# Performance work log

Hardware: AMD Instinct MI355X
Metric: run time of the kernel (lower is better)

Reference implementation:

```python
import jax, jax.numpy as jnp
import numpy as np

H, N, DIN, DOUT = 8, 2048, 768, 1024
HD = DOUT // H
SCALE = 1.0 / float(np.sqrt(HD))
NEG = -1e9
EPS = 1e-5


def setup_inputs() -> dict:
    key = jax.random.key(0)
    ks = jax.random.split(key, 20)
    w = lambda i, shape: jax.random.normal(ks[i], shape, jnp.float32) * 0.02
    inp = {
        'x': jax.random.normal(ks[0], (N, DIN), jnp.float32),
        'batch': jnp.sort(jax.random.randint(ks[1], (N,), 0, 64)).astype(jnp.int64)
                 if jax.config.jax_enable_x64 else jnp.sort(jax.random.randint(ks[1], (N,), 0, 64)),
        'motif_to_atom_attn': jax.random.normal(ks[2], (H, N, N), jnp.float32),
        'wq_w': w(3, (DIN, DOUT)), 'wq_b': jnp.zeros((DOUT,), jnp.float32),
        'wk_w': w(4, (DIN, DOUT)), 'wk_b': jnp.zeros((DOUT,), jnp.float32),
        'wv_w': w(5, (DIN, DOUT)), 'wv_b': jnp.zeros((DOUT,), jnp.float32),
        'wo_w': w(6, (DOUT, DIN)), 'wo_b': jnp.zeros((DIN,), jnp.float32),
        'ln_g': jnp.ones((DIN,), jnp.float32), 'ln_b': jnp.zeros((DIN,), jnp.float32),
        'alpha': jnp.float32(0.5), 'beta': jnp.float32(0.5),
        'gate_q_w': w(7, (DOUT, H)), 'gate_q_b': jnp.zeros((H,), jnp.float32),
        'gate_k_w': w(8, (DOUT, H)), 'gate_k_b': jnp.zeros((H,), jnp.float32),
        'head_interaction': jnp.eye(H, dtype=jnp.float32) + 0.01 * jax.random.normal(ks[9], (H, H), jnp.float32),
    }
    return inp


def reference(x, batch, motif_to_atom_attn, wq_w, wq_b, wk_w, wk_b, wv_w, wv_b,
              wo_w, wo_b, ln_g, ln_b, alpha, beta, gate_q_w, gate_q_b,
              gate_k_w, gate_k_b, head_interaction):
    n = x.shape[0]
    # projections -> [H, N, hd]
    q = (x @ wq_w + wq_b).reshape(n, H, HD).transpose(1, 0, 2)
    k = (x @ wk_w + wk_b).reshape(n, H, HD).transpose(1, 0, 2)
    v = (x @ wv_w + wv_b).reshape(n, H, HD).transpose(1, 0, 2)
    # scaled scores with block-diagonal batch mask [H, N, N]
    scores = jnp.einsum('hid,hjd->hij', q, k) * SCALE
    mask = batch[:, None] == batch[None, :]
    scores = jnp.where(mask[None, :, :], scores, NEG)
    attn_final = scores
    # Guide bias: torch permutes (N,N,H)->permute(2,1,0) which TRANSPOSES node dims
    attn_base = alpha * scores + beta * motif_to_atom_attn          # [H, N, N]
    attn_final = attn_final + jnp.swapaxes(attn_base, 1, 2)        # transposed in (i,j)
    # dynamic gating
    q_flat = q.transpose(1, 0, 2).reshape(n, DOUT)
    k_flat = k.transpose(1, 0, 2).reshape(n, DOUT)
    gq = jnp.tanh(q_flat @ gate_q_w + gate_q_b)                    # [N, H]
    gk = jnp.tanh(k_flat @ gate_k_w + gate_k_b)                    # [N, H]
    attn_final = attn_final + scores * (gq.T[:, :, None] + gk.T[:, None, :])
    # head interaction: res[m,i,j] = sum_h scores[h,i,j] * W[h,m]
    attn_final = attn_final + jnp.einsum('hij,hm->mij', scores, head_interaction)
    probs = jax.nn.softmax(attn_final, axis=-1)
    out = jnp.einsum('hij,hjd->hid', probs, v).transpose(1, 0, 2).reshape(n, DOUT)
    out = out @ wo_w + wo_b
    y = out + x
    mu = jnp.mean(y, axis=-1, keepdims=True)
    var = jnp.mean(jnp.square(y - mu), axis=-1, keepdims=True)
    y = (y - mu) * jax.lax.rsqrt(var + EPS) * ln_g + ln_b
    return y, attn_final
```

## Files before the change

kernel.cpp:

```cpp
#include <hip/hip_runtime.h>

#define NN    2048
#define DIN   768
#define DOUT  1024
#define NH    8
#define HD    128
#define SCALEF 0.08838834764831845f
#define NEGF  (-1.0e9f)
#define EPSF  1e-5f
#define EXPSHIFT 16.0f

typedef __attribute__((ext_vector_type(4))) float f32x4;
typedef __attribute__((ext_vector_type(8))) short bf16x8;

#define OFF_OBF  0
#define OFF_WOT  1048576
#define OFF_YACC 1441792
#define OFF_Q    3686400
#define OFF_K    4734976
#define OFF_VB   5783552
#define OFF_VT   6832128
#define OFF_XB   7880704
#define OFF_WT   8667136
#define OFF_GQ   9846784
#define OFF_GK   9863168

__device__ __forceinline__ short f2bf(float f) {
  union { float f; unsigned u; } v; v.f = f;
  unsigned r = v.u + 0x7FFF + ((v.u >> 16) & 1);
  return (short)(r >> 16);
}
__device__ __forceinline__ float bf2f(short s) {
  union { unsigned u; float f; } v; v.u = ((unsigned)(unsigned short)s) << 16;
  return v.f;
}

__global__ __launch_bounds__(256) void k_prep(const float* __restrict__ x,
                                              short* __restrict__ xb,
                                              const float* __restrict__ wq,
                                              const float* __restrict__ wk,
                                              const float* __restrict__ wv,
                                              short* __restrict__ Wt,
                                              const float* __restrict__ wo,
                                              short* __restrict__ wot) {
  const int bid = blockIdx.x;
  const int tid = threadIdx.x;
  if (bid < 1536) {
    int idx = bid * 256 + tid;
    float4 v = ((const float4*)x)[idx];
    union { short s[4]; float2 f; } u;
    u.s[0] = f2bf(v.x); u.s[1] = f2bf(v.y); u.s[2] = f2bf(v.z); u.s[3] = f2bf(v.w);
    ((float2*)xb)[idx] = u.f;
    return;
  }
  __shared__ float t[64][65];
  if (bid < 2112) {
    const int w = bid - 1536;
    const int z = w / 192, rem = w % 192;
    const int c0 = (rem % 16) * 64, k0 = (rem / 16) * 64;
    const float* Wm = (z == 0) ? wq : (z == 1) ? wk : wv;
#pragma unroll
    for (int l = 0; l < 4; ++l) {
      int f = tid + l * 256;
      int r = f >> 4, c4 = (f & 15) * 4;
      *(float4*)&t[r][c4] = *(const float4*)(Wm + (size_t)(k0 + r) * DOUT + c0 + c4);
    }
    __syncthreads();
    int r2 = tid >> 2, q = tid & 3;
    union { short s[16]; float4 f[2]; } buf;
#pragma unroll
    for (int jj = 0; jj < 16; ++jj) buf.s[jj] = f2bf(t[q * 16 + jj][r2]);
    short* dst = Wt + (size_t)z * (1024 * 768) + (size_t)(c0 + r2) * 768 + k0 + q * 16;
    ((float4*)dst)[0] = buf.f[0];
    ((float4*)dst)[1] = buf.f[1];
  } else {
    const int w = bid - 2112;
    const int c0 = (w % 12) * 64, k0 = (w / 12) * 64;
#pragma unroll
    for (int l = 0; l < 4; ++l) {
      int f = tid + l * 256;
      int r = f >> 4, c4 = (f & 15) * 4;
      *(float4*)&t[r][c4] = *(const float4*)(wo + (size_t)(k0 + r) * DIN + c0 + c4);
    }
    __syncthreads();
    int r2 = tid >> 2, q = tid & 3;
    union { short s[16]; float4 f[2]; } buf;
#pragma unroll
    for (int jj = 0; jj < 16; ++jj) buf.s[jj] = f2bf(t[q * 16 + jj][r2]);
    short* dst = wot + (size_t)(c0 + r2) * DOUT + k0 + q * 16;
    ((float4*)dst)[0] = buf.f[0];
    ((float4*)dst)[1] = buf.f[1];
  }
}

__global__ __launch_bounds__(256) void k_qkv(const short* __restrict__ xb,
                                             const short* __restrict__ Wt,
                                             const float* __restrict__ bq,
                                             const float* __restrict__ bk,
                                             const float* __restrict__ bv,
                                             short* __restrict__ Qb,
                                             short* __restrict__ Kb,
                                             short* __restrict__ Vb) {
  const int n0 = blockIdx.x * 128;
  const int i0 = blockIdx.y * 64;
  const int mat = n0 >> 10;
  const int cl = n0 & 1023;
  const float* bias = (mat == 0) ? bq : (mat == 1) ? bk : bv;
  const short* Wm = Wt + (size_t)mat * (1024 * 768);
  const int tid = threadIdx.x, lane = tid & 63, wave = tid >> 6;
  const int ln = lane & 15, quad = lane >> 4, q8 = quad * 8;
  __shared__ __align__(16) short Bs[2][128][56];
  const int brow = tid >> 1, bseg = (tid & 1) * 16;
  const short* gB = Wm + (size_t)(cl + brow) * DIN + bseg;
  {
    bf16x8 b0 = *(const bf16x8*)(gB);
    bf16x8 b1 = *(const bf16x8*)(gB + 8);
    *(bf16x8*)&Bs[0][brow][bseg] = b0;
    *(bf16x8*)&Bs[0][brow][bseg + 8] = b1;
  }
  bf16x8 cb0 = *(const bf16x8*)(gB + 32);
  bf16x8 cb1 = *(const bf16x8*)(gB + 40);
  __syncthreads();
  f32x4 acc[8];
#pragma unroll
  for (int nt = 0; nt < 8; ++nt) acc[nt] = (f32x4){0.f, 0.f, 0.f, 0.f};
  const short* a0 = xb + (size_t)(i0 + 16 * wave + ln) * DIN + q8;
  for (int ks = 0; ks < 24; ++ks) {
    const int bufc = ks & 1;
    bf16x8 nb0, nb1;
    if (ks < 22) {
      nb0 = *(const bf16x8*)(gB + 32 * (ks + 2));
      nb1 = *(const bf16x8*)(gB + 32 * (ks + 2) + 8);
    }
    bf16x8 A0 = *(const bf16x8*)(a0 + 32 * ks);
#pragma unroll
    for (int nt = 0; nt < 8; ++nt) {
      bf16x8 B = *(const bf16x8*)&Bs[bufc][16 * nt + ln][q8];
      acc[nt] = __builtin_amdgcn_mfma_f32_16x16x32_bf16(A0, B, acc[nt], 0, 0, 0);
    }
    if (ks < 23) {
      *(bf16x8*)&Bs[bufc ^ 1][brow][bseg] = cb0;
      *(bf16x8*)&Bs[bufc ^ 1][brow][bseg + 8] = cb1;
    }
    __syncthreads();
    if (ks < 22) { cb0 = nb0; cb1 = nb1; }
  }
#pragma unroll
  for (int nt = 0; nt < 8; ++nt) {
    int cg = cl + 16 * nt + ln;
    float bb = bias[cg];
#pragma unroll
    for (int reg = 0; reg < 4; ++reg) {
      int rr = i0 + 16 * wave + quad * 4 + reg;
      short s = f2bf(acc[nt][reg] + bb);
      if (mat == 2) {
        Vb[(size_t)rr * 1024 + cg] = s;
      } else {
        int h = cg >> 7, d = cg & 127;
        (mat == 0 ? Qb : Kb)[((size_t)h * NN + rr) * HD + d] = s;
      }
    }
  }
}

__global__ __launch_bounds__(256) void k_vtg(const short* __restrict__ Qb,
                                             const short* __restrict__ Kb,
                                             const float* __restrict__ gqw,
                                             const float* __restrict__ gqb,
                                             const float* __restrict__ gkw,
                                             const float* __restrict__ gkb,
                                             float* __restrict__ GQ,
                                             float* __restrict__ GK,
                                             const short* __restrict__ Vb,
                                             short* __restrict__ Vt) {
  const int bid = blockIdx.x;
  const int tid = threadIdx.x;
  __shared__ __align__(16) char smem[17408];
  if (bid < 2048) {
    const int i = bid;
    const int lane = tid & 63, wave = tid >> 6;
    float aq[NH] = {}, ak[NH] = {};
    for (int d = tid; d < DOUT; d += 256) {
      int h = d >> 7, dd = d & 127;
      float qv = bf2f(Qb[((size_t)h * NN + i) * HD + dd]);
      float kv = bf2f(Kb[((size_t)h * NN + i) * HD + dd]);
      float4 ga = *(const float4*)(gqw + (size_t)d * NH);
      float4 gb = *(const float4*)(gqw + (size_t)d * NH + 4);
      float4 ha = *(const float4*)(gkw + (size_t)d * NH);
      float4 hb = *(const float4*)(gkw + (size_t)d * NH + 4);
      aq[0] = fmaf(qv, ga.x, aq[0]); aq[1] = fmaf(qv, ga.y, aq[1]);
      aq[2] = fmaf(qv, ga.z, aq[2]); aq[3] = fmaf(qv, ga.w, aq[3]);
      aq[4] = fmaf(qv, gb.x, aq[4]); aq[5] = fmaf(qv, gb.y, aq[5]);
      aq[6] = fmaf(qv, gb.z, aq[6]); aq[7] = fmaf(qv, gb.w, aq[7]);
      ak[0] = fmaf(kv, ha.x, ak[0]); ak[1] = fmaf(kv, ha.y, ak[1]);
      ak[2] = fmaf(kv, ha.z, ak[2]); ak[3] = fmaf(kv, ha.w, ak[3]);
      ak[4] = fmaf(kv, hb.x, ak[4]); ak[5] = fmaf(kv, hb.y, ak[5]);
      ak[6] = fmaf(kv, hb.z, ak[6]); ak[7] = fmaf(kv, hb.w, ak[7]);
    }
#pragma unroll
    for (int h = 0; h < NH; ++h) {
#pragma unroll
      for (int off = 1; off < 64; off <<= 1) {
        aq[h] += __shfl_xor(aq[h], off);
        ak[h] += __shfl_xor(ak[h], off);
      }
    }
    auto part = (float (*)[16])(smem);
    if (lane == 0) {
#pragma unroll
      for (int h = 0; h < NH; ++h) {
        part[wave][h] = aq[h];
        part[wave][8 + h] = ak[h];
      }
    }
    __syncthreads();
    if (tid < 16) {
      float s = part[0][tid] + part[1][tid] + part[2][tid] + part[3][tid];
      if (tid < 8) GQ[(size_t)i * NH + tid] = tanhf(s + gqb[tid]);
      else GK[(size_t)i * NH + tid - 8] = tanhf(s + gkb[tid - 8]);
    }
  } else {
    auto t = (short (*)[136])(smem);
    const int w = bid - 2048;
    const int i0 = (w & 31) * 64, h = w >> 5;
#pragma unroll
    for (int l = 0; l < 2; ++l) {
      int f = tid + l * 256;
      int r = f >> 3, c8 = (f & 7) * 16;
      const short* src = Vb + (size_t)(i0 + r) * 1024 + h * HD + c8;
      *(bf16x8*)&t[r][c8] = *(const bf16x8*)src;
      *(bf16x8*)&t[r][c8 + 8] = *(const bf16x8*)(src + 8);
    }
    __syncthreads();
    int d = tid >> 1, half = tid & 1;
    union { short s[32]; float4 f[4]; } buf;
#pragma unroll
    for (int ii = 0; ii < 32; ++ii) buf.s[ii] = t[32 * half + ii][d];
    short* dst = Vt + (size_t)h * (HD * NN) + (size_t)d * NN + i0 + 32 * half;
#pragma unroll
    for (int q = 0; q < 4; ++q) ((float4*)dst)[q] = buf.f[q];
  }
}

__global__ __launch_bounds__(256, 4) void k_sa(const short* __restrict__ Qb,
                                               const short* __restrict__ Kb,
                                               const int* __restrict__ batch,
                                               const float* __restrict__ motif,
                                               const float* __restrict__ GQ,
                                               const float* __restrict__ GK,
                                               const float* __restrict__ Wh,
                                               const float* __restrict__ alpha_p,
                                               const float* __restrict__ beta_p,
                                               float* __restrict__ ATTN) {
  const unsigned gid = blockIdx.y * gridDim.x + blockIdx.x;
  const unsigned xcd = gid & 7, idx = gid >> 3;
  const unsigned P = xcd + 8 * (idx >> 8);
  const unsigned r256 = idx & 255;
  const unsigned bx = 16 * (P & 3) + (r256 & 15);
  const unsigned by = 16 * (P >> 2) + (r256 >> 4);
  const int i0 = by * 32, j0 = bx * 32;

  const int tid = threadIdx.x, lane = tid & 63, wave = tid >> 6;
  const int wr = wave >> 1, wc = wave & 1;
  const int ln = lane & 15, quad = lane >> 4, q8 = quad * 8;

  __shared__ __align__(16) char smem[38400];
  auto Qs  = (short (*)[32][136])(smem);
  auto Ks  = (short (*)[32][136])(smem + 17408);
  auto oL  = (float (*)[36])(smem);
  auto gqL = (float (*)[12])(smem + 34816);
  auto gkL = (float (*)[12])(smem + 36352);
  float* sW = (float*)(smem + 37888);

  const int rA = 16 * wr + quad * 4;
  const int cA = 16 * wc + ln;

  const int srow = tid >> 3, sseg = (tid & 7) * 16;
  const short* gQ0 = Qb + (size_t)(i0 + srow) * HD + sseg;
  const short* gK0 = Kb + (size_t)(j0 + srow) * HD + sseg;
  const size_t hstep = (size_t)NN * HD;

  {
    bf16x8 q0 = *(const bf16x8*)(gQ0);
    bf16x8 q1 = *(const bf16x8*)(gQ0 + 8);
    bf16x8 k0 = *(const bf16x8*)(gK0);
    bf16x8 k1 = *(const bf16x8*)(gK0 + 8);
    *(bf16x8*)&Qs[0][srow][sseg] = q0;
    *(bf16x8*)&Qs[0][srow][sseg + 8] = q1;
    *(bf16x8*)&Ks[0][srow][sseg] = k0;
    *(bf16x8*)&Ks[0][srow][sseg + 8] = k1;
  }
  bf16x8 cq0 = *(const bf16x8*)(gQ0 + hstep);
  bf16x8 cq1 = *(const bf16x8*)(gQ0 + hstep + 8);
  bf16x8 ck0 = *(const bf16x8*)(gK0 + hstep);
  bf16x8 ck1 = *(const bf16x8*)(gK0 + hstep + 8);
  if (tid < 64) {
    const int half = tid >> 5, r = tid & 31;
    const float* src = (half ? GK : GQ) + (size_t)((half ? j0 : i0) + r) * NH;
    float4 a = *(const float4*)src;
    float4 b = *(const float4*)(src + 4);
    float* dst = half ? &gkL[r][0] : &gqL[r][0];
    *(float4*)dst = a;
    *(float4*)(dst + 4) = b;
    sW[tid] = Wh[tid];
  }
  const int4 bi4 = *(const int4*)(batch + i0 + rA);
  const int bj = batch[j0 + cA];
  const float alpha = alpha_p[0], beta = beta_p[0];
  __syncthreads();

  f32x4 accS[NH], accT[NH];
#pragma unroll
  for (int h = 0; h < NH; ++h) {
    accS[h] = (f32x4){0.f, 0.f, 0.f, 0.f};
    accT[h] = (f32x4){0.f, 0.f, 0.f, 0.f};
  }

#pragma unroll
  for (int h = 0; h < NH; ++h) {
    const int bufc = h & 1;
    bf16x8 nq0, nq1, nk0, nk1;
    if (h < 6) {
      const short* gq_ = gQ0 + (size_t)(h + 2) * hstep;
      const short* gk_ = gK0 + (size_t)(h + 2) * hstep;
      nq0 = *(const bf16x8*)(gq_);
      nq1 = *(const bf16x8*)(gq_ + 8);
      nk0 = *(const bf16x8*)(gk_);
      nk1 = *(const bf16x8*)(gk_ + 8);
    }
#pragma unroll
    for (int ks = 0; ks < 4; ++ks) {
      bf16x8 aS = *(const bf16x8*)&Qs[bufc][16 * wr + ln][ks * 32 + q8];
      bf16x8 bS = *(const bf16x8*)&Ks[bufc][16 * wc + ln][ks * 32 + q8];
      accS[h] = __builtin_amdgcn_mfma_f32_16x16x32_bf16(aS, bS, accS[h], 0, 0, 0);
      bf16x8 aT = *(const bf16x8*)&Ks[bufc][16 * wr + ln][ks * 32 + q8];
      bf16x8 bT = *(const bf16x8*)&Qs[bufc][16 * wc + ln][ks * 32 + q8];
      accT[h] = __builtin_amdgcn_mfma_f32_16x16x32_bf16(aT, bT, accT[h], 0, 0, 0);
    }
    if (h < 7) {
      *(bf16x8*)&Qs[bufc ^ 1][srow][sseg] = cq0;
      *(bf16x8*)&Qs[bufc ^ 1][srow][sseg + 8] = cq1;
      *(bf16x8*)&Ks[bufc ^ 1][srow][sseg] = ck0;
      *(bf16x8*)&Ks[bufc ^ 1][srow][sseg + 8] = ck1;
    }
    __syncthreads();
    if (h < 6) { cq0 = nq0; cq1 = nq1; ck0 = nk0; ck1 = nk1; }
  }

  int okm[4];
  okm[0] = (bi4.x == bj); okm[1] = (bi4.y == bj);
  okm[2] = (bi4.z == bj); okm[3] = (bi4.w == bj);
#pragma unroll
  for (int reg = 0; reg < 4; ++reg)
#pragma unroll
    for (int h = 0; h < NH; ++h)
      accS[h][reg] = okm[reg] ? accS[h][reg] * SCALEF : NEGF;

  const int orow = tid >> 3, oslot = (tid & 7) * 4;
  union { float4 v; float f[4]; } moc, mon, mo2;
  moc.v = *(const float4*)(motif + ((size_t)(j0 + cA)) * NN + i0 + rA);
  mon.v = *(const float4*)(motif + ((size_t)(NN + j0 + cA)) * NN + i0 + rA);
#pragma unroll
  for (int h = 0; h < NH; ++h) {
    if (h < 6)
      mo2.v = *(const float4*)(motif + ((size_t)(h + 2) * NN + j0 + cA) * NN + i0 + rA);
    float w8[NH];
#pragma unroll
    for (int h2 = 0; h2 < NH; ++h2) w8[h2] = sW[h2 * NH + h];
    const float gkj = gkL[cA][h];
#pragma unroll
    for (int reg = 0; reg < 4; ++reg) {
      float tv = okm[reg] ? accT[h][reg] * SCALEF : NEGF;
      float hm = 0.f;
#pragma unroll
      for (int h2 = 0; h2 < NH; ++h2) hm = fmaf(accS[h2][reg], w8[h2], hm);
      float o = accS[h][reg] * (1.f + gqL[rA + reg][h] + gkj) +
                alpha * tv + beta * moc.f[reg] + hm;
      oL[rA + reg][cA] = o;
    }
    __syncthreads();
    float4 ov = *(const float4*)&oL[orow][oslot];
    *(float4*)(ATTN + ((size_t)h * NN + i0 + orow) * NN + j0 + oslot) = ov;
    if (h < 7) __syncthreads();
    moc.v = mon.v;
    mon.v = mo2.v;
  }
}

__global__ __launch_bounds__(256) void k_pv(const float* __restrict__ ATTN,
                                            const short* __restrict__ Vt,
                                            short* __restrict__ Obf) {
  const int bid = blockIdx.x;
  const int h = bid & 7;
  const int i0 = (bid >> 3) * 16;
  const int tid = threadIdx.x, lane = tid & 63, wave = tid >> 6;
  const int ln = lane & 15, quad = lane >> 4, q8 = quad * 8;
  __shared__ float accL[4][16][140];
  __shared__ float SUML[4][16];
  const int jbase = wave * 512;
  const float* arow = ATTN + ((size_t)h * NN + i0 + ln) * NN + jbase;
  const short* vbase = Vt + (size_t)h * (HD * NN) + jbase;
  f32x4 acc[8];
#pragma unroll
  for (int nt = 0; nt < 8; ++nt) acc[nt] = (f32x4){0.f, 0.f, 0.f, 0.f};
  float rowsum = 0.f;
  for (int c = 0; c < 16; ++c) {
    const int jk = c * 32;
    float4 u1 = *(const float4*)(arow + jk + q8);
    float4 u2 = *(const float4*)(arow + jk + q8 + 4);
    float p0 = __expf(u1.x - EXPSHIFT), p1 = __expf(u1.y - EXPSHIFT);
    float p2 = __expf(u1.z - EXPSHIFT), p3 = __expf(u1.w - EXPSHIFT);
    float p4 = __expf(u2.x - EXPSHIFT), p5 = __expf(u2.y - EXPSHIFT);
    float p6 = __expf(u2.z - EXPSHIFT), p7 = __expf(u2.w - EXPSHIFT);
    rowsum += ((p0 + p1) + (p2 + p3)) + ((p4 + p5) + (p6 + p7));
    bf16x8 a;
    a[0] = f2bf(p0); a[1] = f2bf(p1); a[2] = f2bf(p2); a[3] = f2bf(p3);
    a[4] = f2bf(p4); a[5] = f2bf(p5); a[6] = f2bf(p6); a[7] = f2bf(p7);
#pragma unroll
    for (int nt = 0; nt < 8; ++nt) {
      bf16x8 b = *(const bf16x8*)(vbase + (size_t)(16 * nt + ln) * NN + jk + q8);
      acc[nt] = __builtin_amdgcn_mfma_f32_16x16x32_bf16(a, b, acc[nt], 0, 0, 0);
    }
  }
  rowsum += __shfl_xor(rowsum, 16);
  rowsum += __shfl_xor(rowsum, 32);
  if (lane < 16) SUML[wave][ln] = rowsum;
#pragma unroll
  for (int nt = 0; nt < 8; ++nt)
#pragma unroll
    for (int reg = 0; reg < 4; ++reg)
      accL[wave][quad * 4 + reg][16 * nt + ln] = acc[nt][reg];
  __syncthreads();
  const int r = tid >> 4, d0 = (tid & 15) * 8;
  const float inv = 1.0f / (SUML[0][r] + SUML[1][r] + SUML[2][r] + SUML[3][r]);
  union { short s[8]; bf16x8 v; } ob;
#pragma unroll
  for (int e = 0; e < 8; ++e) {
    float s = accL[0][r][d0 + e] + accL[1][r][d0 + e] +
              accL[2][r][d0 + e] + accL[3][r][d0 + e];
    ob.s[e] = f2bf(s * inv);
  }
  *(bf16x8*)(Obf + (size_t)(i0 + r) * DOUT + h * HD + d0) = ob.v;
}

__global__ __launch_bounds__(256) void k_outproj(const short* __restrict__ Obf,
                                                 const short* __restrict__ wot,
                                                 float* __restrict__ YACC) {
  const int n0 = blockIdx.x * 64;
  const int i0 = blockIdx.y * 64;
  const int tid = threadIdx.x, lane = tid & 63, wave = tid >> 6;
  const int ln = lane & 15, quad = lane >> 4, q8 = quad * 8;
  __shared__ __align__(16) short Bs[2][64][56];
  const int brow = tid >> 2, bseg = (tid & 3) * 8;
  const short* gB = wot + (size_t)(n0 + brow) * DOUT + bseg;
  {
    bf16x8 b0 = *(const bf16x8*)(gB);
    *(bf16x8*)&Bs[0][brow][bseg] = b0;
  }
  bf16x8 cb0 = *(const bf16x8*)(gB + 32);
  __syncthreads();
  f32x4 acc[4];
#pragma unroll
  for (int nt = 0; nt < 4; ++nt) acc[nt] = (f32x4){0.f, 0.f, 0.f, 0.f};
  const short* a0 = Obf + (size_t)(i0 + 16 * wave + ln) * DOUT + q8;
  for (int ks = 0; ks < 32; ++ks) {
    const int bufc = ks & 1;
    bf16x8 nb0;
    if (ks < 30) nb0 = *(const bf16x8*)(gB + 32 * (ks + 2));
    bf16x8 A0 = *(const bf16x8*)(a0 + 32 * ks);
#pragma unroll
    for (int nt = 0; nt < 4; ++nt) {
      bf16x8 B = *(const bf16x8*)&Bs[bufc][16 * nt + ln][q8];
      acc[nt] = __builtin_amdgcn_mfma_f32_16x16x32_bf16(A0, B, acc[nt], 0, 0, 0);
    }
    if (ks < 31) *(bf16x8*)&Bs[bufc ^ 1][brow][bseg] = cb0;
    __syncthreads();
    if (ks < 30) cb0 = nb0;
  }
#pragma unroll
  for (int nt = 0; nt < 4; ++nt) {
    int cg = n0 + 16 * nt + ln;
#pragma unroll
    for (int reg = 0; reg < 4; ++reg) {
      int rr = i0 + 16 * wave + quad * 4 + reg;
      YACC[(size_t)rr * DIN + cg] = acc[nt][reg];
    }
  }
}

__global__ __launch_bounds__(256) void k_ln(const float* __restrict__ YACC,
                                            const float* __restrict__ x,
                                            const float* __restrict__ wo_b,
                                            const float* __restrict__ g,
                                            const float* __restrict__ b,
                                            float* __restrict__ y) {
  const int i = blockIdx.x;
  const int tid = threadIdx.x;
  const int lane = tid & 63, wave = tid >> 6;
  float v[3];
#pragma unroll
  for (int t = 0; t < 3; ++t) {
    int cc = tid + t * 256;
    v[t] = YACC[(size_t)i * DIN + cc] + wo_b[cc] + x[(size_t)i * DIN + cc];
  }
  __shared__ float p1[4], p2[4];
  float s = v[0] + v[1] + v[2];
#pragma unroll
  for (int off = 1; off < 64; off <<= 1) s += __shfl_xor(s, off);
  if (lane == 0) p1[wave] = s;
  __syncthreads();
  const float mu = (p1[0] + p1[1] + p1[2] + p1[3]) * (1.0f / DIN);
  float q = 0.f;
#pragma unroll
  for (int t = 0; t < 3; ++t) {
    float d = v[t] - mu;
    q += d * d;
  }
#pragma unroll
  for (int off = 1; off < 64; off <<= 1) q += __shfl_xor(q, off);
  if (lane == 0) p2[wave] = q;
  __syncthreads();
  const float rs = rsqrtf((p2[0] + p2[1] + p2[2] + p2[3]) * (1.0f / DIN) + EPSF);
#pragma unroll
  for (int t = 0; t < 3; ++t) {
    int cc = tid + t * 256;
    y[(size_t)i * DIN + cc] = (v[t] - mu) * rs * g[cc] + b[cc];
  }
}

extern "C" void kernel_launch(void* const* d_in, const int* in_sizes, int n_in,
                              void* d_out, int out_size, void* d_ws, size_t ws_size,
                              hipStream_t stream) {
  (void)in_sizes; (void)n_in; (void)out_size; (void)ws_size;
  const float* x       = (const float*)d_in[0];
  const int*   batch   = (const int*)d_in[1];
  const float* motif   = (const float*)d_in[2];
  const float* wq_w    = (const float*)d_in[3];
  const float* wq_b    = (const float*)d_in[4];
  const float* wk_w    = (const float*)d_in[5];
  const float* wk_b    = (const float*)d_in[6];
  const float* wv_w    = (const float*)d_in[7];
  const float* wv_b    = (const float*)d_in[8];
  const float* wo_w    = (const float*)d_in[9];
  const float* wo_b    = (const float*)d_in[10];
  const float* ln_g    = (const float*)d_in[11];
  const float* ln_b    = (const float*)d_in[12];
  const float* alpha_p = (const float*)d_in[13];
  const float* beta_p  = (const float*)d_in[14];
  const float* gq_w    = (const float*)d_in[15];
  const float* gq_b    = (const float*)d_in[16];
  const float* gk_w    = (const float*)d_in[17];
  const float* gk_b    = (const float*)d_in[18];
  const float* headW   = (const float*)d_in[19];

  float* y    = (float*)d_out;
  float* ATTN = (float*)d_out + (size_t)NN * DIN;
  float* ws   = (float*)d_ws;
  short* Obf  = (short*)(ws + OFF_OBF);
  short* wot  = (short*)(ws + OFF_WOT);
  float* YACC = ws + OFF_YACC;
  short* Qb   = (short*)(ws + OFF_Q);
  short* Kb   = (short*)(ws + OFF_K);
  short* Vb   = (short*)(ws + OFF_VB);
  short* Vt   = (short*)(ws + OFF_VT);
  short* xb   = (short*)(ws + OFF_XB);
  short* Wt   = (short*)(ws + OFF_WT);
  float* GQ   = ws + OFF_GQ;
  float* GK   = ws + OFF_GK;

  k_prep<<<2304, 256, 0, stream>>>(x, xb, wq_w, wk_w, wv_w, Wt, wo_w, wot);
  k_qkv<<<dim3(24, 32), 256, 0, stream>>>(xb, Wt, wq_b, wk_b, wv_b, Qb, Kb, Vb);
  k_vtg<<<2304, 256, 0, stream>>>(Qb, Kb, gq_w, gq_b, gk_w, gk_b, GQ, GK, Vb, Vt);
  k_sa<<<dim3(64, 64), 256, 0, stream>>>(Qb, Kb, batch, motif, GQ, GK, headW,
                                         alpha_p, beta_p, ATTN);
  k_pv<<<1024, 256, 0, stream>>>(ATTN, Vt, Obf);
  k_outproj<<<dim3(12, 32), 256, 0, stream>>>(Obf, wot, YACC);
  k_ln<<<NN, 256, 0, stream>>>(YACC, x, wo_b, ln_g, ln_b, y);
}
```

Baseline: 454.5 us.

## Single-buffer k_sa LDS for higher occupancy and prefetch V/attn in k_pv

k_sa drops its double-buffered Q/K shared memory tiles in favour of a single buffer with an extra barrier per head. This roughly halves LDS use and raises the launch bound to 6 blocks per CU, trading pipelining for occupancy. k_pv now software-pipelines its loop by loading the next chunk's V fragments and attention scores into registers before the current chunk's exp and MFMA work, with full unroll and a 4-block launch bound. The goal is to hide global memory latency, at the cost of more register pressure and an extra sync in k_sa.

```diff
diff --git a/kernel.cpp b/kernel.cpp
--- a/kernel.cpp
+++ b/kernel.cpp
@@ -242,7 +242,7 @@
   }
 }
 
-__global__ __launch_bounds__(256, 4) void k_sa(const short* __restrict__ Qb,
+__global__ __launch_bounds__(256, 6) void k_sa(const short* __restrict__ Qb,
                                                const short* __restrict__ Kb,
                                                const int* __restrict__ batch,
                                                const float* __restrict__ motif,
@@ -264,13 +264,13 @@
   const int wr = wave >> 1, wc = wave & 1;
   const int ln = lane & 15, quad = lane >> 4, q8 = quad * 8;
 
-  __shared__ __align__(16) char smem[38400];
-  auto Qs  = (short (*)[32][136])(smem);
-  auto Ks  = (short (*)[32][136])(smem + 17408);
+  __shared__ __align__(16) char smem[20736];
+  auto Qs  = (short (*)[136])(smem);
+  auto Ks  = (short (*)[136])(smem + 8704);
   auto oL  = (float (*)[36])(smem);
-  auto gqL = (float (*)[12])(smem + 34816);
-  auto gkL = (float (*)[12])(smem + 36352);
-  float* sW = (float*)(smem + 37888);
+  auto gqL = (float (*)[12])(smem + 17408);
+  auto gkL = (float (*)[12])(smem + 18944);
+  float* sW = (float*)(smem + 20480);
 
   const int rA = 16 * wr + quad * 4;
   const int cA = 16 * wc + ln;
@@ -285,10 +285,10 @@
     bf16x8 q1 = *(const bf16x8*)(gQ0 + 8);
     bf16x8 k0 = *(const bf16x8*)(gK0);
     bf16x8 k1 = *(const bf16x8*)(gK0 + 8);
-    *(bf16x8*)&Qs[0][srow][sseg] = q0;
-    *(bf16x8*)&Qs[0][srow][sseg + 8] = q1;
-    *(bf16x8*)&Ks[0][srow][sseg] = k0;
-    *(bf16x8*)&Ks[0][srow][sseg + 8] = k1;
+    *(bf16x8*)&Qs[srow][sseg] = q0;
+    *(bf16x8*)&Qs[srow][sseg + 8] = q1;
+    *(bf16x8*)&Ks[srow][sseg] = k0;
+    *(bf16x8*)&Ks[srow][sseg + 8] = k1;
   }
   bf16x8 cq0 = *(const bf16x8*)(gQ0 + hstep);
   bf16x8 cq1 = *(const bf16x8*)(gQ0 + hstep + 8);
@@ -318,7 +318,6 @@
 
 #pragma unroll
   for (int h = 0; h < NH; ++h) {
-    const int bufc = h & 1;
     bf16x8 nq0, nq1, nk0, nk1;
     if (h < 6) {
       const short* gq_ = gQ0 + (size_t)(h + 2) * hstep;
@@ -330,20 +329,21 @@
     }
 #pragma unroll
     for (int ks = 0; ks < 4; ++ks) {
-      bf16x8 aS = *(const bf16x8*)&Qs[bufc][16 * wr + ln][ks * 32 + q8];
-      bf16x8 bS = *(const bf16x8*)&Ks[bufc][16 * wc + ln][ks * 32 + q8];
+      bf16x8 aS = *(const bf16x8*)&Qs[16 * wr + ln][ks * 32 + q8];
+      bf16x8 bS = *(const bf16x8*)&Ks[16 * wc + ln][ks * 32 + q8];
       accS[h] = __builtin_amdgcn_mfma_f32_16x16x32_bf16(aS, bS, accS[h], 0, 0, 0);
-      bf16x8 aT = *(const bf16x8*)&Ks[bufc][16 * wr + ln][ks * 32 + q8];
-      bf16x8 bT = *(const bf16x8*)&Qs[bufc][16 * wc + ln][ks * 32 + q8];
+      bf16x8 aT = *(const bf16x8*)&Ks[16 * wr + ln][ks * 32 + q8];
+      bf16x8 bT = *(const bf16x8*)&Qs[16 * wc + ln][ks * 32 + q8];
       accT[h] = __builtin_amdgcn_mfma_f32_16x16x32_bf16(aT, bT, accT[h], 0, 0, 0);
     }
+    __syncthreads();
     if (h < 7) {
-      *(bf16x8*)&Qs[bufc ^ 1][srow][sseg] = cq0;
-      *(bf16x8*)&Qs[bufc ^ 1][srow][sseg + 8] = cq1;
-      *(bf16x8*)&Ks[bufc ^ 1][srow][sseg] = ck0;
-      *(bf16x8*)&Ks[bufc ^ 1][srow][sseg + 8] = ck1;
-    }
-    __syncthreads();
+      *(bf16x8*)&Qs[srow][sseg] = cq0;
+      *(bf16x8*)&Qs[srow][sseg + 8] = cq1;
+      *(bf16x8*)&Ks[srow][sseg] = ck0;
+      *(bf16x8*)&Ks[srow][sseg + 8] = ck1;
+      __syncthreads();
+    }
     if (h < 6) { cq0 = nq0; cq1 = nq1; ck0 = nk0; ck1 = nk1; }
   }
 
@@ -387,9 +387,9 @@
   }
 }
 
-__global__ __launch_bounds__(256) void k_pv(const float* __restrict__ ATTN,
-                                            const short* __restrict__ Vt,
-                                            short* __restrict__ Obf) {
+__global__ __launch_bounds__(256, 4) void k_pv(const float* __restrict__ ATTN,
+                                               const short* __restrict__ Vt,
+                                               short* __restrict__ Obf) {
   const int bid = blockIdx.x;
   const int h = bid & 7;
   const int i0 = (bid >> 3) * 16;
@@ -404,10 +404,24 @@
 #pragma unroll
   for (int nt = 0; nt < 8; ++nt) acc[nt] = (f32x4){0.f, 0.f, 0.f, 0.f};
   float rowsum = 0.f;
+  bf16x8 vc[8];
+#pragma unroll
+  for (int nt = 0; nt < 8; ++nt)
+    vc[nt] = *(const bf16x8*)(vbase + (size_t)(16 * nt + ln) * NN + q8);
+  float4 u1 = *(const float4*)(arow + q8);
+  float4 u2 = *(const float4*)(arow + q8 + 4);
+#pragma unroll
   for (int c = 0; c < 16; ++c) {
     const int jk = c * 32;
-    float4 u1 = *(const float4*)(arow + jk + q8);
-    float4 u2 = *(const float4*)(arow + jk + q8 + 4);
+    bf16x8 vn[8];
+    float4 n1, n2;
+    if (c < 15) {
+#pragma unroll
+      for (int nt = 0; nt < 8; ++nt)
+        vn[nt] = *(const bf16x8*)(vbase + (size_t)(16 * nt + ln) * NN + jk + 32 + q8);
+      n1 = *(const float4*)(arow + jk + 32 + q8);
+      n2 = *(const float4*)(arow + jk + 32 + q8 + 4);
+    }
     float p0 = __expf(u1.x - EXPSHIFT), p1 = __expf(u1.y - EXPSHIFT);
     float p2 = __expf(u1.z - EXPSHIFT), p3 = __expf(u1.w - EXPSHIFT);
     float p4 = __expf(u2.x - EXPSHIFT), p5 = __expf(u2.y - EXPSHIFT);
@@ -417,9 +431,12 @@
     a[0] = f2bf(p0); a[1] = f2bf(p1); a[2] = f2bf(p2); a[3] = f2bf(p3);
     a[4] = f2bf(p4); a[5] = f2bf(p5); a[6] = f2bf(p6); a[7] = f2bf(p7);
 #pragma unroll
-    for (int nt = 0; nt < 8; ++nt) {
-      bf16x8 b = *(const bf16x8*)(vbase + (size_t)(16 * nt + ln) * NN + jk + q8);
-      acc[nt] = __builtin_amdgcn_mfma_f32_16x16x32_bf16(a, b, acc[nt], 0, 0, 0);
+    for (int nt = 0; nt < 8; ++nt)
+      acc[nt] = __builtin_amdgcn_mfma_f32_16x16x32_bf16(a, vc[nt], acc[nt], 0, 0, 0);
+    if (c < 15) {
+#pragma unroll
+      for (int nt = 0; nt < 8; ++nt) vc[nt] = vn[nt];
+      u1 = n1; u2 = n2;
     }
   }
   rowsum += __shfl_xor(rowsum, 16);
```

New measurement: 513.1 us. 12.9% more time.
